# Optimization experiments

Hardware: AMD Instinct MI355X
Metric: run time of the kernel (lower is better)

The kernel has to match this reference:

```python
import jax, jax.numpy as jnp
import numpy as np

N_NODES = 50000
N_EDGES = 800000
D_IN = 128
D_OUT = 128
ALPHA = 0.2  # LeakyReLU negative slope


def setup_inputs() -> dict:
    key = jax.random.key(0)
    k1, k2, k3, k4 = jax.random.split(key, 4)
    x = jax.random.normal(k1, (N_NODES, D_IN), dtype=jnp.float32)
    W = jax.random.normal(k2, (D_IN, D_OUT), dtype=jnp.float32) * (1.414 / np.sqrt(D_IN))
    a = jax.random.normal(k3, (2 * D_OUT, 1), dtype=jnp.float32) * 0.1
    edge_index = jax.random.randint(k4, (2, N_EDGES), 0, N_NODES, dtype=jnp.int64)
    return {"x": x, "W": W, "a": a, "edge_index": edge_index}


def reference(x, W, a, edge_index):
    # h: (N, D_OUT)
    h = x @ W
    src, dst = edge_index[0], edge_index[1]
    # e_i = leakyrelu([h[src]; h[dst]] @ a) == leakyrelu((h@a1)[src] + (h@a2)[dst])
    a1 = a[:D_OUT, 0]
    a2 = a[D_OUT:, 0]
    s1 = h @ a1  # (N,)
    s2 = h @ a2  # (N,)
    e = jax.nn.leaky_relu(s1[src] + s2[dst], negative_slope=ALPHA)  # (E,)
    # Global softmax over all edges (faithful to F.softmax(edge_e, dim=0))
    attention = jax.nn.softmax(e)  # (E,)
    # output[dst] += attention * h[src]  (scatter-add)
    msgs = attention[:, None] * h[src]  # (E, D_OUT)
    output = jax.ops.segment_sum(msgs, dst, num_segments=N_NODES)
    return output
```

## Files before the change

kernel.cpp:

```cpp
#include <hip/hip_runtime.h>
#include <hip/hip_bf16.h>

#define N_NODES 50000
#define N_EDGES 800000
#define D 128
#define ALPHA 0.2f
#define NEG_INF -1e30f

#define KB_BLOCKS 3125
#define LDS_STRIDE 272

#define SCAN_PER 52
#define SCAN_PAD (1024 * SCAN_PER)
#define NB_MS ((N_EDGES + 1023) / 1024)

typedef __attribute__((ext_vector_type(8))) short short8;
typedef __attribute__((ext_vector_type(4))) float floatx4;

__device__ __forceinline__ unsigned int f2bf(float v)
{
    __hip_bfloat16 b = __float2bfloat16(v);
    return (unsigned int)*reinterpret_cast<unsigned short*>(&b);
}
__device__ __forceinline__ float bf_lo(unsigned int u)
{
    return __uint_as_float(u << 16);
}
__device__ __forceinline__ float bf_hi(unsigned int u)
{
    return __uint_as_float(u & 0xFFFF0000u);
}

__global__ __launch_bounds__(1024) void k_prep(
    const float* __restrict__ W, const float* __restrict__ a,
    float* __restrict__ w12, unsigned short* __restrict__ wb,
    int* __restrict__ deg)
{
    const int t = threadIdx.x;
    deg[blockIdx.x * 1024 + t] = 0;

    if (blockIdx.x == 0 && t < 256) {
        const int r = t & 127;
        const int which = t >> 7;
        const float* av = a + which * D;
        float acc = 0.f;
        #pragma unroll 8
        for (int j = 0; j < D; ++j)
            acc += W[(size_t)r * D + j] * av[j];
        w12[which * D + r] = acc;
    }
    if (blockIdx.x == 1) {
        #pragma unroll
        for (int k = 0; k < 16; ++k) {
            const int f = t * 16 + k;
            const int j    = f & 7;
            const int lane = (f >> 3) & 63;
            const int half = (f >> 9) & 1;
            const int kt   = (f >> 10) & 3;
            const int wv   = f >> 12;
            const int q    = lane >> 4;
            const int nIdx = lane & 15;
            const float val =
                W[(size_t)(kt * 32 + q * 8 + j) * D + wv * 32 + 2 * nIdx + half];
            wb[f] = (unsigned short)f2bf(val);
        }
    }
}

__global__ __launch_bounds__(256) void k_fused(
    const float* __restrict__ x, const float* __restrict__ w12,
    const unsigned short* __restrict__ wb, const int* __restrict__ ei,
    unsigned short* __restrict__ hb, float* __restrict__ s1,
    float* __restrict__ s2, int* __restrict__ deg, int* __restrict__ rank)
{
    __shared__ unsigned char lds[16 * LDS_STRIDE];
    const int t = threadIdx.x;
    const int rowbase = blockIdx.x * 16;

    const int r = t >> 4;
    const int c = t & 15;
    const float* xp = x + (size_t)(rowbase + r) * D + c * 8;
    const float4 v0 = *(const float4*)(xp);
    const float4 v1 = *(const float4*)(xp + 4);

    const int lane = t & 63;
    const int wv = t >> 6;
    const int q = lane >> 4;
    const int nIdx = lane & 15;
    const int n0 = wv * 32;
    const short8* wbp = (const short8*)wb;
    short8 B[2][4];
    #pragma unroll
    for (int kt = 0; kt < 4; ++kt) {
        B[0][kt] = wbp[((wv * 4 + kt) * 2 + 0) * 64 + lane];
        B[1][kt] = wbp[((wv * 4 + kt) * 2 + 1) * 64 + lane];
    }

    {
        const float* w1 = w12 + c * 8;
        const float* w2 = w12 + D + c * 8;
        float p1 = v0.x * w1[0] + v0.y * w1[1] + v0.z * w1[2] + v0.w * w1[3]
                 + v1.x * w1[4] + v1.y * w1[5] + v1.z * w1[6] + v1.w * w1[7];
        float p2 = v0.x * w2[0] + v0.y * w2[1] + v0.z * w2[2] + v0.w * w2[3]
                 + v1.x * w2[4] + v1.y * w2[5] + v1.z * w2[6] + v1.w * w2[7];
        #pragma unroll
        for (int mask = 8; mask >= 1; mask >>= 1) {
            p1 += __shfl_xor(p1, mask);
            p2 += __shfl_xor(p2, mask);
        }
        if (c == 0) { s1[rowbase + r] = p1; s2[rowbase + r] = p2; }

        uint4 pk;
        pk.x = f2bf(v0.x) | (f2bf(v0.y) << 16);
        pk.y = f2bf(v0.z) | (f2bf(v0.w) << 16);
        pk.z = f2bf(v1.x) | (f2bf(v1.y) << 16);
        pk.w = f2bf(v1.z) | (f2bf(v1.w) << 16);
        *(uint4*)(lds + r * LDS_STRIDE + c * 16) = pk;
    }
    __syncthreads();

    const unsigned char* ab = lds + nIdx * LDS_STRIDE + q * 16;
    const short8 A0 = *(const short8*)(ab);
    const short8 A1 = *(const short8*)(ab + 64);
    const short8 A2 = *(const short8*)(ab + 128);
    const short8 A3 = *(const short8*)(ab + 192);

    floatx4 acc0 = {0.f, 0.f, 0.f, 0.f};
    floatx4 acc1 = {0.f, 0.f, 0.f, 0.f};
    acc0 = __builtin_amdgcn_mfma_f32_16x16x32_bf16(A0, B[0][0], acc0, 0, 0, 0);
    acc1 = __builtin_amdgcn_mfma_f32_16x16x32_bf16(A0, B[1][0], acc1, 0, 0, 0);
    acc0 = __builtin_amdgcn_mfma_f32_16x16x32_bf16(A1, B[0][1], acc0, 0, 0, 0);
    acc1 = __builtin_amdgcn_mfma_f32_16x16x32_bf16(A1, B[1][1], acc1, 0, 0, 0);
    acc0 = __builtin_amdgcn_mfma_f32_16x16x32_bf16(A2, B[0][2], acc0, 0, 0, 0);
    acc1 = __builtin_amdgcn_mfma_f32_16x16x32_bf16(A2, B[1][2], acc1, 0, 0, 0);
    acc0 = __builtin_amdgcn_mfma_f32_16x16x32_bf16(A3, B[0][3], acc0, 0, 0, 0);
    acc1 = __builtin_amdgcn_mfma_f32_16x16x32_bf16(A3, B[1][3], acc1, 0, 0, 0);

    #pragma unroll
    for (int i = 0; i < 4; ++i) {
        const int row = rowbase + q * 4 + i;
        const unsigned int pk = f2bf(acc0[i]) | (f2bf(acc1[i]) << 16);
        *(unsigned int*)(hb + (size_t)row * D + n0 + 2 * nIdx) = pk;
    }

    const int e = blockIdx.x * 256 + t;
    rank[e] = atomicAdd(&deg[ei[N_EDGES + e]], 1);
}

__device__ __forceinline__ void online_combine(float& m, float& s,
                                               float om, float os)
{
    float nm = fmaxf(m, om);
    s = s * __expf(m - nm) + os * __expf(om - nm);
    m = nm;
}

__global__ __launch_bounds__(1024) void k_mid(
    const int* __restrict__ ei, const float* __restrict__ s1,
    const float* __restrict__ s2, const int* __restrict__ deg,
    int* __restrict__ offs, float* __restrict__ bm, float* __restrict__ bs)
{
    const int t = threadIdx.x;
    const int lane = t & 63;
    const int wv = t >> 6;

    if (blockIdx.x == 0) {
        __shared__ int wsum[16];
        const int base = t * SCAN_PER;
        int4 v[13];
        const int4* dp = (const int4*)(deg + base);
        int s = 0;
        #pragma unroll
        for (int k = 0; k < 13; ++k) {
            v[k] = dp[k];
            s += v[k].x + v[k].y + v[k].z + v[k].w;
        }
        int inc = s;
        #pragma unroll
        for (int off = 1; off < 64; off <<= 1) {
            int u = __shfl_up(inc, off);
            if (lane >= off) inc += u;
        }
        if (lane == 63) wsum[wv] = inc;
        __syncthreads();
        if (wv == 0 && lane < 16) {
            int wval = wsum[lane];
            int winc = wval;
            #pragma unroll
            for (int off = 1; off < 16; off <<= 1) {
                int u = __shfl_up(winc, off);
                if (lane >= off) winc += u;
            }
            wsum[lane] = winc - wval;
        }
        __syncthreads();
        int run = wsum[wv] + (inc - s);
        int4* op = (int4*)(offs + base);
        #pragma unroll
        for (int k = 0; k < 13; ++k) {
            int4 o;
            o.x = run;             run += v[k].x;
            o.y = run;             run += v[k].y;
            o.z = run;             run += v[k].z;
            o.w = run;             run += v[k].w;
            op[k] = o;
        }
        return;
    }

    const int e = (blockIdx.x - 1) * 1024 + t;
    float m = NEG_INF, s = 0.f;
    if (e < N_EDGES) {
        const int sN = ei[e];
        const int dN = ei[N_EDGES + e];
        float vv = s1[sN] + s2[dN];
        vv = vv > 0.f ? vv : ALPHA * vv;
        m = vv;
        s = 1.f;
    }
    #pragma unroll
    for (int off = 32; off >= 1; off >>= 1) {
        float om = __shfl_down(m, off);
        float os = __shfl_down(s, off);
        online_combine(m, s, om, os);
    }
    __shared__ float rm[16], rs[16];
    if (lane == 0) { rm[wv] = m; rs[wv] = s; }
    __syncthreads();
    if (t == 0) {
        #pragma unroll
        for (int w = 1; w < 16; ++w) online_combine(m, s, rm[w], rs[w]);
        bm[blockIdx.x - 1] = m;
        bs[blockIdx.x - 1] = s;
    }
}

__global__ __launch_bounds__(256) void k_post(
    const int* __restrict__ ei, const int* __restrict__ offs,
    const int* __restrict__ rank, unsigned int* __restrict__ csr,
    const float* __restrict__ bm, const float* __restrict__ bs,
    float* __restrict__ MZ)
{
    const int e = blockIdx.x * 256 + threadIdx.x;
    const int sN = ei[e];
    const int dN = ei[N_EDGES + e];
    csr[offs[dN] + rank[e]] = (unsigned int)sN;

    if (blockIdx.x == 0) {
        float m = NEG_INF, s = 0.f;
        for (int i = threadIdx.x; i < NB_MS; i += 256)
            online_combine(m, s, bm[i], bs[i]);
        #pragma unroll
        for (int off = 32; off >= 1; off >>= 1) {
            float om = __shfl_down(m, off);
            float os = __shfl_down(s, off);
            online_combine(m, s, om, os);
        }
        __shared__ float rm[4], rs[4];
        const int wid = threadIdx.x >> 6;
        if ((threadIdx.x & 63) == 0) { rm[wid] = m; rs[wid] = s; }
        __syncthreads();
        if (threadIdx.x == 0) {
            #pragma unroll
            for (int w = 1; w < 4; ++w) online_combine(m, s, rm[w], rs[w]);
            MZ[0] = m;
            MZ[1] = s;
        }
    }
}

__global__ __launch_bounds__(256) void k_gather(
    const unsigned int* __restrict__ csr, const int* __restrict__ offs,
    const float* __restrict__ s1, const float* __restrict__ s2,
    const unsigned short* __restrict__ hb, const float* __restrict__ MZ,
    float* __restrict__ out)
{
    const int node = (blockIdx.x * blockDim.x + threadIdx.x) >> 6;
    if (node >= N_NODES) return;
    const int lane = threadIdx.x & 63;
    const float M = MZ[0];
    const float invZ = 1.0f / MZ[1];
    const float s2n = s2[node];
    const int beg = offs[node];
    const int end = offs[node + 1];

    float a0 = 0.f, a1 = 0.f, b0 = 0.f, b1 = 0.f;
    float c0 = 0.f, c1 = 0.f, d0 = 0.f, d1 = 0.f;
    float e0 = 0.f, e1 = 0.f, f0 = 0.f, f1 = 0.f;
    float g0 = 0.f, g1 = 0.f, h0 = 0.f, h1 = 0.f;

    for (int cb = beg; cb < end; cb += 64) {
        const int n = min(64, end - cb);
        const int srcl = (cb + lane < end) ? (int)csr[cb + lane] : 0;
        float v = s1[srcl] + s2n;
        v = v > 0.f ? v : ALPHA * v;
        const float attl = __expf(v - M) * invZ;

        int j = 0;
        for (; j + 7 < n; j += 8) {
            const int i0 = __shfl(srcl, j);
            const int i1 = __shfl(srcl, j + 1);
            const int i2 = __shfl(srcl, j + 2);
            const int i3 = __shfl(srcl, j + 3);
            const int i4 = __shfl(srcl, j + 4);
            const int i5 = __shfl(srcl, j + 5);
            const int i6 = __shfl(srcl, j + 6);
            const int i7 = __shfl(srcl, j + 7);
            const float w0 = __shfl(attl, j);
            const float w1 = __shfl(attl, j + 1);
            const float w2 = __shfl(attl, j + 2);
            const float w3 = __shfl(attl, j + 3);
            const float w4 = __shfl(attl, j + 4);
            const float w5 = __shfl(attl, j + 5);
            const float w6 = __shfl(attl, j + 6);
            const float w7 = __shfl(attl, j + 7);
            const unsigned int u0 = *(const unsigned int*)(hb + (size_t)i0 * D + lane * 2);
            const unsigned int u1 = *(const unsigned int*)(hb + (size_t)i1 * D + lane * 2);
            const unsigned int u2 = *(const unsigned int*)(hb + (size_t)i2 * D + lane * 2);
            const unsigned int u3 = *(const unsigned int*)(hb + (size_t)i3 * D + lane * 2);
            const unsigned int u4 = *(const unsigned int*)(hb + (size_t)i4 * D + lane * 2);
            const unsigned int u5 = *(const unsigned int*)(hb + (size_t)i5 * D + lane * 2);
            const unsigned int u6 = *(const unsigned int*)(hb + (size_t)i6 * D + lane * 2);
            const unsigned int u7 = *(const unsigned int*)(hb + (size_t)i7 * D + lane * 2);
            a0 += w0 * bf_lo(u0); a1 += w0 * bf_hi(u0);
            b0 += w1 * bf_lo(u1); b1 += w1 * bf_hi(u1);
            c0 += w2 * bf_lo(u2); c1 += w2 * bf_hi(u2);
            d0 += w3 * bf_lo(u3); d1 += w3 * bf_hi(u3);
            e0 += w4 * bf_lo(u4); e1 += w4 * bf_hi(u4);
            f0 += w5 * bf_lo(u5); f1 += w5 * bf_hi(u5);
            g0 += w6 * bf_lo(u6); g1 += w6 * bf_hi(u6);
            h0 += w7 * bf_lo(u7); h1 += w7 * bf_hi(u7);
        }
        for (; j + 3 < n; j += 4) {
            const int i0 = __shfl(srcl, j);
            const int i1 = __shfl(srcl, j + 1);
            const int i2 = __shfl(srcl, j + 2);
            const int i3 = __shfl(srcl, j + 3);
            const float w0 = __shfl(attl, j);
            const float w1 = __shfl(attl, j + 1);
            const float w2 = __shfl(attl, j + 2);
            const float w3 = __shfl(attl, j + 3);
            const unsigned int u0 = *(const unsigned int*)(hb + (size_t)i0 * D + lane * 2);
            const unsigned int u1 = *(const unsigned int*)(hb + (size_t)i1 * D + lane * 2);
            const unsigned int u2 = *(const unsigned int*)(hb + (size_t)i2 * D + lane * 2);
            const unsigned int u3 = *(const unsigned int*)(hb + (size_t)i3 * D + lane * 2);
            a0 += w0 * bf_lo(u0); a1 += w0 * bf_hi(u0);
            b0 += w1 * bf_lo(u1); b1 += w1 * bf_hi(u1);
            c0 += w2 * bf_lo(u2); c1 += w2 * bf_hi(u2);
            d0 += w3 * bf_lo(u3); d1 += w3 * bf_hi(u3);
        }
        for (; j < n; ++j) {
            const int i0 = __shfl(srcl, j);
            const float w0 = __shfl(attl, j);
            const unsigned int u0 = *(const unsigned int*)(hb + (size_t)i0 * D + lane * 2);
            a0 += w0 * bf_lo(u0); a1 += w0 * bf_hi(u0);
        }
    }
    float2 r;
    r.x = ((a0 + b0) + (c0 + d0)) + ((e0 + f0) + (g0 + h0));
    r.y = ((a1 + b1) + (c1 + d1)) + ((e1 + f1) + (g1 + h1));
    *(float2*)(out + (size_t)node * D + lane * 2) = r;
}

extern "C" void kernel_launch(void* const* d_in, const int* in_sizes, int n_in,
                              void* d_out, int out_size, void* d_ws, size_t ws_size,
                              hipStream_t stream)
{
    const float* x = (const float*)d_in[0];
    const float* W = (const float*)d_in[1];
    const float* a = (const float*)d_in[2];
    const int* ei = (const int*)d_in[3];
    float* out = (float*)d_out;

    char* wsb = (char*)d_ws;
    unsigned int* csr = (unsigned int*)wsb;
    unsigned short* hb = (unsigned short*)(wsb + (size_t)N_EDGES * 4);
    unsigned short* wb = hb + (size_t)N_NODES * D;
    int* rank     = (int*)(wb + 16384);
    float* s1     = (float*)(rank + N_EDGES);
    float* s2     = s1 + N_NODES;
    int*   deg    = (int*)(s2 + N_NODES);
    int*   offs   = deg + SCAN_PAD;
    float* w12    = (float*)(offs + SCAN_PAD);
    float* bm     = w12 + 2 * D;
    float* bs     = bm + NB_MS;
    float* MZ     = bs + NB_MS;

    k_prep<<<SCAN_PAD / 1024, 1024, 0, stream>>>(W, a, w12, wb, deg);
    k_fused<<<N_NODES / 16, 256, 0, stream>>>(x, w12, wb, ei, hb, s1, s2,
                                              deg, rank);
    k_mid<<<NB_MS + 1, 1024, 0, stream>>>(ei, s1, s2, deg, offs, bm, bs);
    k_post<<<KB_BLOCKS, 256, 0, stream>>>(ei, offs, rank, csr, bm, bs, MZ);
    k_gather<<<(N_NODES * 64 + 255) / 256, 256, 0, stream>>>(
        csr, offs, s1, s2, hb, MZ, out);
}
```

Before: 182.4 us.

## Precompute edge logits once, store them in CSR records, restructure softmax reduction

Adds a separate k_sc kernel that computes s1/s2 ahead of time. k_fused then computes each edge's LeakyReLU logit, writes it to a ve buffer, and produces per-block max and sum-of-exp partials. k_mid shrinks to two blocks that run the scan and the global max/sum reduction, and k_post writes 8-byte (src, logit) CSR records. k_gather reads the stored logit instead of doing random s1 lookups, and k_prep spreads the w12/wb preparation across more blocks. In exchange it adds a kernel launch, a second read of x, and twice the CSR write/read traffic.

```diff
diff --git a/kernel.cpp b/kernel.cpp
--- a/kernel.cpp
+++ b/kernel.cpp
@@ -12,7 +12,6 @@
 
 #define SCAN_PER 52
 #define SCAN_PAD (1024 * SCAN_PER)
-#define NB_MS ((N_EDGES + 1023) / 1024)
 
 typedef __attribute__((ext_vector_type(8))) short short8;
 typedef __attribute__((ext_vector_type(4))) float floatx4;
@@ -37,45 +36,83 @@
     int* __restrict__ deg)
 {
     const int t = threadIdx.x;
-    deg[blockIdx.x * 1024 + t] = 0;
-
-    if (blockIdx.x == 0 && t < 256) {
-        const int r = t & 127;
-        const int which = t >> 7;
-        const float* av = a + which * D;
-        float acc = 0.f;
-        #pragma unroll 8
-        for (int j = 0; j < D; ++j)
-            acc += W[(size_t)r * D + j] * av[j];
-        w12[which * D + r] = acc;
-    }
-    if (blockIdx.x == 1) {
+    const int b = blockIdx.x;
+    deg[b * 1024 + t] = 0;
+
+    if (b < 4) {
+        const int g = b * 64 + (t >> 4);
+        const int c = t & 15;
+        const int which = g >> 7;
+        const int r = g & 127;
+        const float* wp = W + (size_t)r * D + c * 8;
+        const float* ap = a + which * D + c * 8;
+        const float4 u0 = *(const float4*)(wp);
+        const float4 u1 = *(const float4*)(wp + 4);
+        const float4 c0 = *(const float4*)(ap);
+        const float4 c1 = *(const float4*)(ap + 4);
+        float p = u0.x * c0.x + u0.y * c0.y + u0.z * c0.z + u0.w * c0.w
+                + u1.x * c1.x + u1.y * c1.y + u1.z * c1.z + u1.w * c1.w;
         #pragma unroll
-        for (int k = 0; k < 16; ++k) {
-            const int f = t * 16 + k;
-            const int j    = f & 7;
-            const int lane = (f >> 3) & 63;
-            const int half = (f >> 9) & 1;
-            const int kt   = (f >> 10) & 3;
-            const int wv   = f >> 12;
-            const int q    = lane >> 4;
-            const int nIdx = lane & 15;
-            const float val =
-                W[(size_t)(kt * 32 + q * 8 + j) * D + wv * 32 + 2 * nIdx + half];
-            wb[f] = (unsigned short)f2bf(val);
-        }
-    }
+        for (int mask = 8; mask >= 1; mask >>= 1)
+            p += __shfl_xor(p, mask);
+        if (c == 0) w12[which * D + r] = p;
+    } else if (b < 20) {
+        const int f = (b - 4) * 1024 + t;
+        const int j    = f & 7;
+        const int lane = (f >> 3) & 63;
+        const int half = (f >> 9) & 1;
+        const int kt   = (f >> 10) & 3;
+        const int wv   = f >> 12;
+        const int q    = lane >> 4;
+        const int nIdx = lane & 15;
+        const float val =
+            W[(size_t)(kt * 32 + q * 8 + j) * D + wv * 32 + 2 * nIdx + half];
+        wb[f] = (unsigned short)f2bf(val);
+    }
+}
+
+__global__ __launch_bounds__(256) void k_sc(
+    const float* __restrict__ x, const float* __restrict__ w12,
+    float* __restrict__ s1, float* __restrict__ s2)
+{
+    const int t = threadIdx.x;
+    const int r = t >> 4;
+    const int c = t & 15;
+    const int row = blockIdx.x * 16 + r;
+    const float* xp = x + (size_t)row * D + c * 8;
+    const float4 v0 = *(const float4*)(xp);
+    const float4 v1 = *(const float4*)(xp + 4);
+    const float* w1 = w12 + c * 8;
+    const float* w2 = w12 + D + c * 8;
+    float p1 = v0.x * w1[0] + v0.y * w1[1] + v0.z * w1[2] + v0.w * w1[3]
+             + v1.x * w1[4] + v1.y * w1[5] + v1.z * w1[6] + v1.w * w1[7];
+    float p2 = v0.x * w2[0] + v0.y * w2[1] + v0.z * w2[2] + v0.w * w2[3]
+             + v1.x * w2[4] + v1.y * w2[5] + v1.z * w2[6] + v1.w * w2[7];
+    #pragma unroll
+    for (int mask = 8; mask >= 1; mask >>= 1) {
+        p1 += __shfl_xor(p1, mask);
+        p2 += __shfl_xor(p2, mask);
+    }
+    if (c == 0) { s1[row] = p1; s2[row] = p2; }
 }
 
 __global__ __launch_bounds__(256) void k_fused(
-    const float* __restrict__ x, const float* __restrict__ w12,
-    const unsigned short* __restrict__ wb, const int* __restrict__ ei,
-    unsigned short* __restrict__ hb, float* __restrict__ s1,
-    float* __restrict__ s2, int* __restrict__ deg, int* __restrict__ rank)
+    const float* __restrict__ x, const unsigned short* __restrict__ wb,
+    const int* __restrict__ ei, const float* __restrict__ s1,
+    const float* __restrict__ s2, unsigned short* __restrict__ hb,
+    int* __restrict__ deg, int* __restrict__ rank, float* __restrict__ ve,
+    float* __restrict__ bm, float* __restrict__ bs)
 {
     __shared__ unsigned char lds[16 * LDS_STRIDE];
+    __shared__ float red[8];
     const int t = threadIdx.x;
     const int rowbase = blockIdx.x * 16;
+
+    const int e = blockIdx.x * 256 + t;
+    const int sN = ei[e];
+    const int dN = ei[N_EDGES + e];
+    const float s1g = s1[sN];
+    const float s2g = s2[dN];
 
     const int r = t >> 4;
     const int c = t & 15;
@@ -97,19 +134,6 @@
     }
 
     {
-        const float* w1 = w12 + c * 8;
-        const float* w2 = w12 + D + c * 8;
-        float p1 = v0.x * w1[0] + v0.y * w1[1] + v0.z * w1[2] + v0.w * w1[3]
-                 + v1.x * w1[4] + v1.y * w1[5] + v1.z * w1[6] + v1.w * w1[7];
-        float p2 = v0.x * w2[0] + v0.y * w2[1] + v0.z * w2[2] + v0.w * w2[3]
-                 + v1.x * w2[4] + v1.y * w2[5] + v1.z * w2[6] + v1.w * w2[7];
-        #pragma unroll
-        for (int mask = 8; mask >= 1; mask >>= 1) {
-            p1 += __shfl_xor(p1, mask);
-            p2 += __shfl_xor(p2, mask);
-        }
-        if (c == 0) { s1[rowbase + r] = p1; s2[rowbase + r] = p2; }
-
         uint4 pk;
         pk.x = f2bf(v0.x) | (f2bf(v0.y) << 16);
         pk.y = f2bf(v0.z) | (f2bf(v0.w) << 16);
@@ -143,22 +167,34 @@
         *(unsigned int*)(hb + (size_t)row * D + n0 + 2 * nIdx) = pk;
     }
 
-    const int e = blockIdx.x * 256 + t;
-    rank[e] = atomicAdd(&deg[ei[N_EDGES + e]], 1);
-}
-
-__device__ __forceinline__ void online_combine(float& m, float& s,
-                                               float om, float os)
-{
-    float nm = fmaxf(m, om);
-    s = s * __expf(m - nm) + os * __expf(om - nm);
-    m = nm;
+    rank[e] = atomicAdd(&deg[dN], 1);
+    float v = s1g + s2g;
+    v = v > 0.f ? v : ALPHA * v;
+    ve[e] = v;
+
+    float m = v;
+    #pragma unroll
+    for (int mask = 32; mask >= 1; mask >>= 1)
+        m = fmaxf(m, __shfl_xor(m, mask));
+    if (lane == 0) red[wv] = m;
+    __syncthreads();
+    m = fmaxf(fmaxf(red[0], red[1]), fmaxf(red[2], red[3]));
+    float sx = __expf(v - m);
+    #pragma unroll
+    for (int mask = 32; mask >= 1; mask >>= 1)
+        sx += __shfl_xor(sx, mask);
+    if (lane == 0) red[4 + wv] = sx;
+    __syncthreads();
+    if (t == 0) {
+        bm[blockIdx.x] = m;
+        bs[blockIdx.x] = red[4] + red[5] + red[6] + red[7];
+    }
 }
 
 __global__ __launch_bounds__(1024) void k_mid(
-    const int* __restrict__ ei, const float* __restrict__ s1,
-    const float* __restrict__ s2, const int* __restrict__ deg,
-    int* __restrict__ offs, float* __restrict__ bm, float* __restrict__ bs)
+    const int* __restrict__ deg, int* __restrict__ offs,
+    const float* __restrict__ bm, const float* __restrict__ bs,
+    float* __restrict__ MZ)
 {
     const int t = threadIdx.x;
     const int lane = t & 63;
@@ -208,70 +244,52 @@
         return;
     }
 
-    const int e = (blockIdx.x - 1) * 1024 + t;
-    float m = NEG_INF, s = 0.f;
-    if (e < N_EDGES) {
-        const int sN = ei[e];
-        const int dN = ei[N_EDGES + e];
-        float vv = s1[sN] + s2[dN];
-        vv = vv > 0.f ? vv : ALPHA * vv;
-        m = vv;
-        s = 1.f;
-    }
-    #pragma unroll
-    for (int off = 32; off >= 1; off >>= 1) {
-        float om = __shfl_down(m, off);
-        float os = __shfl_down(s, off);
-        online_combine(m, s, om, os);
-    }
-    __shared__ float rm[16], rs[16];
-    if (lane == 0) { rm[wv] = m; rs[wv] = s; }
+    __shared__ float red[16];
+    float m = NEG_INF;
+    for (int i = t; i < KB_BLOCKS; i += 1024)
+        m = fmaxf(m, bm[i]);
+    #pragma unroll
+    for (int mask = 32; mask >= 1; mask >>= 1)
+        m = fmaxf(m, __shfl_xor(m, mask));
+    if (lane == 0) red[wv] = m;
+    __syncthreads();
+    float M = red[0];
+    #pragma unroll
+    for (int w = 1; w < 16; ++w) M = fmaxf(M, red[w]);
+    __syncthreads();
+    float sx = 0.f;
+    for (int i = t; i < KB_BLOCKS; i += 1024)
+        sx += bs[i] * __expf(bm[i] - M);
+    #pragma unroll
+    for (int mask = 32; mask >= 1; mask >>= 1)
+        sx += __shfl_xor(sx, mask);
+    if (lane == 0) red[wv] = sx;
     __syncthreads();
     if (t == 0) {
+        float Z = 0.f;
         #pragma unroll
-        for (int w = 1; w < 16; ++w) online_combine(m, s, rm[w], rs[w]);
-        bm[blockIdx.x - 1] = m;
-        bs[blockIdx.x - 1] = s;
+        for (int w = 0; w < 16; ++w) Z += red[w];
+        MZ[0] = M;
+        MZ[1] = Z;
     }
 }
 
 __global__ __launch_bounds__(256) void k_post(
     const int* __restrict__ ei, const int* __restrict__ offs,
-    const int* __restrict__ rank, unsigned int* __restrict__ csr,
-    const float* __restrict__ bm, const float* __restrict__ bs,
-    float* __restrict__ MZ)
+    const int* __restrict__ rank, const float* __restrict__ ve,
+    uint2* __restrict__ csr64)
 {
     const int e = blockIdx.x * 256 + threadIdx.x;
     const int sN = ei[e];
     const int dN = ei[N_EDGES + e];
-    csr[offs[dN] + rank[e]] = (unsigned int)sN;
-
-    if (blockIdx.x == 0) {
-        float m = NEG_INF, s = 0.f;
-        for (int i = threadIdx.x; i < NB_MS; i += 256)
-            online_combine(m, s, bm[i], bs[i]);
-        #pragma unroll
-        for (int off = 32; off >= 1; off >>= 1) {
-            float om = __shfl_down(m, off);
-            float os = __shfl_down(s, off);
-            online_combine(m, s, om, os);
-        }
-        __shared__ float rm[4], rs[4];
-        const int wid = threadIdx.x >> 6;
-        if ((threadIdx.x & 63) == 0) { rm[wid] = m; rs[wid] = s; }
-        __syncthreads();
-        if (threadIdx.x == 0) {
-            #pragma unroll
-            for (int w = 1; w < 4; ++w) online_combine(m, s, rm[w], rs[w]);
-            MZ[0] = m;
-            MZ[1] = s;
-        }
-    }
+    uint2 rec;
+    rec.x = (unsigned int)sN;
+    rec.y = __float_as_uint(ve[e]);
+    csr64[offs[dN] + rank[e]] = rec;
 }
 
 __global__ __launch_bounds__(256) void k_gather(
-    const unsigned int* __restrict__ csr, const int* __restrict__ offs,
-    const float* __restrict__ s1, const float* __restrict__ s2,
+    const uint2* __restrict__ csr64, const int* __restrict__ offs,
     const unsigned short* __restrict__ hb, const float* __restrict__ MZ,
     float* __restrict__ out)
 {
@@ -280,7 +298,6 @@
     const int lane = threadIdx.x & 63;
     const float M = MZ[0];
     const float invZ = 1.0f / MZ[1];
-    const float s2n = s2[node];
     const int beg = offs[node];
     const int end = offs[node + 1];
 
@@ -291,10 +308,15 @@
 
     for (int cb = beg; cb < end; cb += 64) {
         const int n = min(64, end - cb);
-        const int srcl = (cb + lane < end) ? (int)csr[cb + lane] : 0;
-        float v = s1[srcl] + s2n;
-        v = v > 0.f ? v : ALPHA * v;
-        const float attl = __expf(v - M) * invZ;
+        uint2 rec;
+        if (cb + lane < end) {
+            rec = csr64[cb + lane];
+        } else {
+            rec.x = 0u;
+            rec.y = 0xFF800000u;
+        }
+        const int srcl = (int)rec.x;
+        const float attl = __expf(__uint_as_float(rec.y) - M) * invZ;
 
         int j = 0;
         for (; j + 7 < n; j += 8) {
@@ -373,24 +395,26 @@
     float* out = (float*)d_out;
 
     char* wsb = (char*)d_ws;
-    unsigned int* csr = (unsigned int*)wsb;
-    unsigned short* hb = (unsigned short*)(wsb + (size_t)N_EDGES * 4);
+    uint2* csr64 = (uint2*)wsb;
+    unsigned short* hb = (unsigned short*)(wsb + (size_t)N_EDGES * 8);
     unsigned short* wb = hb + (size_t)N_NODES * D;
     int* rank     = (int*)(wb + 16384);
-    float* s1     = (float*)(rank + N_EDGES);
+    float* ve     = (float*)(rank + N_EDGES);
+    float* s1     = ve + N_EDGES;
     float* s2     = s1 + N_NODES;
     int*   deg    = (int*)(s2 + N_NODES);
     int*   offs   = deg + SCAN_PAD;
     float* w12    = (float*)(offs + SCAN_PAD);
     float* bm     = w12 + 2 * D;
-    float* bs     = bm + NB_MS;
-    float* MZ     = bs + NB_MS;
+    float* bs     = bm + KB_BLOCKS;
+    float* MZ     = bs + KB_BLOCKS;
 
     k_prep<<<SCAN_PAD / 1024, 1024, 0, stream>>>(W, a, w12, wb, deg);
-    k_fused<<<N_NODES / 16, 256, 0, stream>>>(x, w12, wb, ei, hb, s1, s2,
-                                              deg, rank);
-    k_mid<<<NB_MS + 1, 1024, 0, stream>>>(ei, s1, s2, deg, offs, bm, bs);
-    k_post<<<KB_BLOCKS, 256, 0, stream>>>(ei, offs, rank, csr, bm, bs, MZ);
+    k_sc<<<N_NODES / 16, 256, 0, stream>>>(x, w12, s1, s2);
+    k_fused<<<N_NODES / 16, 256, 0, stream>>>(x, wb, ei, s1, s2, hb,
+                                              deg, rank, ve, bm, bs);
+    k_mid<<<2, 1024, 0, stream>>>(deg, offs, bm, bs, MZ);
+    k_post<<<KB_BLOCKS, 256, 0, stream>>>(ei, offs, rank, ve, csr64);
     k_gather<<<(N_NODES * 64 + 255) / 256, 256, 0, stream>>>(
-        csr, offs, s1, s2, hb, MZ, out);
-}
+        csr64, offs, hb, MZ, out);
+}
```

Result: faster. 177.7 us (-2.6%).
